# Kernel tuning notes

Hardware: AMD Instinct MI355X
Metric: run time of the kernel (lower is better)

The kernel has to match this reference:

```python
import jax, jax.numpy as jnp
import numpy as np

EMBED = 1024
D_FF = 4 * EMBED
N_EXPERTS = 8
TOP_K = 2
B, S = 2, 1024


def setup_inputs() -> dict:
    key = jax.random.key(0)
    ks = jax.random.split(key, 10)
    sc_d = 1.0 / np.sqrt(EMBED)
    sc_h = 1.0 / np.sqrt(D_FF)
    return {
        "inputs": jax.random.normal(ks[0], (B, S, EMBED), jnp.float32),
        # router MLP: Linear(D,4D) -> ReLU -> Linear(4D,E)
        "rw1": jax.random.normal(ks[1], (EMBED, D_FF), jnp.float32) * sc_d,
        "rb1": jnp.zeros((D_FF,), jnp.float32),
        "rw2": jax.random.normal(ks[2], (D_FF, N_EXPERTS), jnp.float32) * sc_h,
        "rb2": jnp.zeros((N_EXPERTS,), jnp.float32),
        # stacked expert weights: Linear(D,4D) -> ReLU -> Linear(4D,D)
        "W1": jax.random.normal(ks[3], (N_EXPERTS, EMBED, D_FF), jnp.float32) * sc_d,
        "b1": jnp.zeros((N_EXPERTS, D_FF), jnp.float32),
        "W2": jax.random.normal(ks[4], (N_EXPERTS, D_FF, EMBED), jnp.float32) * sc_h,
        "b2": jnp.zeros((N_EXPERTS, EMBED), jnp.float32),
    }


def reference(inputs, rw1, rb1, rw2, rb2, W1, b1, W2, b2):
    Bb, Ss, D = inputs.shape
    T = Bb * Ss
    xf = inputs.reshape(T, D)  # [T, D]

    # Router: scores over experts, keep top-k, softmax over kept entries only.
    score = jax.nn.relu(xf @ rw1 + rb1) @ rw2 + rb2          # [T, E]
    _, topi = jax.lax.top_k(score, TOP_K)                    # [T, K]
    mask = jnp.zeros(score.shape, bool).at[jnp.arange(T)[:, None], topi].set(True)
    gate = jax.nn.softmax(jnp.where(mask, score, -jnp.inf), axis=-1)  # [T, E]

    # Dense per-expert MLP weighted by gate; gate==0 for non-top-k experts,
    # matching the original masked gather/scatter exactly.
    out = jnp.zeros_like(xf)
    for e in range(N_EXPERTS):
        h = jax.nn.relu(xf @ W1[e] + b1[e])                  # [T, 4D]
        y = h @ W2[e] + b2[e]                                # [T, D]
        out = out + gate[:, e:e + 1] * y
    return out.reshape(Bb, Ss, D)
```

## Files before the change

kernel.cpp:

```cpp
#include <hip/hip_runtime.h>
#include <stdint.h>

typedef unsigned short ushort_t;
typedef __attribute__((ext_vector_type(8))) short short8;
typedef __attribute__((ext_vector_type(4))) float f32x4;

#define EMBED   1024
#define DFF     4096
#define NEXP    8
#define TOKENS  2048
#define SLOTS   4096
#define TMAX    40

__device__ __forceinline__ ushort_t f2bf(float f) {
  unsigned u = __float_as_uint(f);
  u += 0x7FFFu + ((u >> 16) & 1u);
  return (ushort_t)(u >> 16);
}
__device__ __forceinline__ float bf2f(ushort_t b) {
  return __uint_as_float(((unsigned)b) << 16);
}

__device__ __forceinline__ void gl2lds16(const void* g, void* l) {
  typedef const __attribute__((address_space(1))) unsigned char* gp_t;
  typedef __attribute__((address_space(3))) unsigned char* lp_t;
  __builtin_amdgcn_global_load_lds((gp_t)(uintptr_t)g, (lp_t)(uintptr_t)l, 16, 0, 0);
}

__global__ void zero_small(int* counts, int* cursors) {
  int i = threadIdx.x;
  if (i < NEXP) { counts[i] = 0; cursors[i] = 0; }
}

__global__ void split_xhl(const float* __restrict__ x, ushort_t* __restrict__ Xs) {
  int t = blockIdx.x;
  int d = threadIdx.x * 4;
  float4 v = *(const float4*)(x + (size_t)t * EMBED + d);
  ushort4 hi, lo;
  hi.x = f2bf(v.x); lo.x = f2bf(v.x - bf2f(hi.x));
  hi.y = f2bf(v.y); lo.y = f2bf(v.y - bf2f(hi.y));
  hi.z = f2bf(v.z); lo.z = f2bf(v.z - bf2f(hi.z));
  hi.w = f2bf(v.w); lo.w = f2bf(v.w - bf2f(hi.w));
  ushort_t* row = Xs + (size_t)t * 2048;
  *(ushort4*)(row + d)        = hi;
  *(ushort4*)(row + 1024 + d) = lo;
}

__global__ void transp_conv(const float* __restrict__ src, ushort_t* __restrict__ dst,
                            int src_ld, int dst_ld, long src_estride, long dst_estride,
                            int dst_koff, int lo)
{
  __shared__ float t[64][65];
  const float* s = src + (size_t)blockIdx.z * src_estride;
  ushort_t* d = dst + (size_t)blockIdx.z * dst_estride;
  int n0 = blockIdx.x * 64, k0 = blockIdx.y * 64;
  int tid = threadIdx.x;
  int kk = tid >> 4, nn = (tid & 15) * 4;
  #pragma unroll
  for (int it = 0; it < 4; it++) {
    float4 v = *(const float4*)(s + (size_t)(k0 + kk + it * 16) * src_ld + n0 + nn);
    t[kk + it * 16][nn]     = v.x;
    t[kk + it * 16][nn + 1] = v.y;
    t[kk + it * 16][nn + 2] = v.z;
    t[kk + it * 16][nn + 3] = v.w;
  }
  __syncthreads();
  int nn2 = tid >> 3, kk2 = (tid & 7) * 8;
  #pragma unroll
  for (int it = 0; it < 2; it++) {
    int n = nn2 + it * 32;
    union { ushort_t u[8]; uint4 v; } pk;
    #pragma unroll
    for (int j = 0; j < 8; j++) {
      float xv = t[kk2 + j][n];
      ushort_t hv = f2bf(xv);
      pk.u[j] = lo ? f2bf(xv - bf2f(hv)) : hv;
    }
    *(uint4*)(d + (size_t)(n0 + n) * dst_ld + dst_koff + k0 + kk2) = pk.v;
  }
}

template<int APATH, int OUTMODE, bool RELU, bool EXPERT, int SPLITK, int NX>
__global__ __launch_bounds__(256, 3)
void gemm_kernel(const ushort_t* __restrict__ A, const ushort_t* __restrict__ B,
                 const float* __restrict__ bias, void* __restrict__ Cout,
                 const float* __restrict__ slot_gate, const int* __restrict__ slot_token,
                 const int* __restrict__ off, const int* __restrict__ tile_e,
                 const int* __restrict__ tile_y, int e0, int e1,
                 int M, int N, int K)
{
  __shared__ ushort_t As[2][128 * 32];
  __shared__ ushort_t Bs[2][128 * 32];

  int e = 0, kc = 0, row0, col0, m_base, m_cnt;
  if (EXPERT) {
    int bid  = blockIdx.x;
    int xi   = bid % NX;
    int rest = bid / NX;
    kc       = rest % SPLITK;
    int t    = rest / SPLITK;
    e = tile_e[t];
    if (e < e0 || e >= e1) return;
    row0   = tile_y[t] * 128;
    col0   = xi * 128;
    m_base = off[e];
    m_cnt  = off[e + 1] - m_base;
  } else {
    row0 = blockIdx.y * 128;
    col0 = blockIdx.x * 128;
    m_base = 0; m_cnt = M;
    if (row0 >= m_cnt) return;
  }
  const int Kc   = K / SPLITK;
  const int kbeg = kc * Kc;

  const int tid  = threadIdx.x;
  const int lane = tid & 63;
  const int wid  = tid >> 6;
  const int wm = wid & 1, wn = wid >> 1;

  const int srow  = lane >> 2;
  const int schk8 = ((lane & 3) ^ ((lane >> 3) & 3)) * 8;

  const ushort_t* gA[2];
  const ushort_t* gB[2];
  int aoff[2];
  const ushort_t* Bt = B + (EXPERT ? (size_t)(e - e0) * (size_t)N * K : 0);
  #pragma unroll
  for (int h = 0; h < 2; h++) {
    int r  = row0 + h * 64 + wid * 16 + srow;
    int rl = min(r, m_cnt - 1);
    size_t rowb;
    if (APATH == 2)      rowb = (size_t)slot_token[m_base + rl] * 2048;
    else if (APATH == 1) rowb = (size_t)rl * 2048;
    else                 rowb = (size_t)(m_base + rl) * (size_t)K;
    gA[h]   = A + rowb + (APATH == 0 ? kbeg : 0) + schk8;
    aoff[h] = (h * 64 + wid * 16) * 32;

    int n = col0 + h * 64 + wid * 16 + srow;
    gB[h] = Bt + (size_t)n * K + kbeg + schk8;
  }

  auto stage = [&](int pb, int k0) {
    const int k0a = (APATH == 1 && k0 >= 2048) ? k0 - 2048 : k0;
    #pragma unroll
    for (int h = 0; h < 2; h++) {
      gl2lds16(gA[h] + k0a, &As[pb][aoff[h]]);
      gl2lds16(gB[h] + k0,  &Bs[pb][aoff[h]]);
    }
  };

  f32x4 acc[4][4];
  #pragma unroll
  for (int i = 0; i < 4; i++)
    #pragma unroll
    for (int j = 0; j < 4; j++)
      acc[i][j] = (f32x4){0.f, 0.f, 0.f, 0.f};

  const int q  = lane >> 4;
  const int rr = lane & 15;
  const int sw8 = (q ^ ((rr >> 1) & 3)) * 8;
  const int abase = (wm * 64 + rr) * 32 + sw8;
  const int bbase = (wn * 64 + rr) * 32 + sw8;

  const int nkt = Kc >> 5;

  stage(0, 0);
  __syncthreads();

  for (int kt = 0; kt < nkt; kt++) {
    const int cur = kt & 1, nxt = cur ^ 1;
    if (kt + 1 < nkt) stage(nxt, (kt + 1) << 5);

    short8 af[4], bfr[4];
    #pragma unroll
    for (int i = 0; i < 4; i++) {
      af[i]  = *(const short8*)(&As[cur][abase + i * 512]);
      bfr[i] = *(const short8*)(&Bs[cur][bbase + i * 512]);
    }
    #pragma unroll
    for (int mt = 0; mt < 4; mt++)
      #pragma unroll
      for (int nt = 0; nt < 4; nt++)
        acc[mt][nt] = __builtin_amdgcn_mfma_f32_16x16x32_bf16(af[mt], bfr[nt], acc[mt][nt], 0, 0, 0);

    __syncthreads();
  }

  const float* biasp = bias + (EXPERT ? (size_t)e * N : 0);
  float bv[4];
  #pragma unroll
  for (int nt = 0; nt < 4; nt++)
    bv[nt] = biasp[col0 + wn * 64 + nt * 16 + rr];
  const float bscale = (SPLITK == 1 || kc == 0) ? 1.f : 0.f;

  if constexpr (OUTMODE == 4) {
    const float* rw2p = slot_gate;
    float4 wa[4], wb[4];
    #pragma unroll
    for (int nt = 0; nt < 4; nt++) {
      int c = col0 + wn * 64 + nt * 16 + rr;
      wa[nt] = *(const float4*)(rw2p + (size_t)c * 8);
      wb[nt] = *(const float4*)(rw2p + (size_t)c * 8 + 4);
    }
    float* Ps = (float*)Cout;
    const int xi2 = (col0 >> 6) + wn;
    #pragma unroll
    for (int mt = 0; mt < 4; mt++) {
      #pragma unroll
      for (int i = 0; i < 4; i++) {
        float4 sA = {0.f, 0.f, 0.f, 0.f}, sB = {0.f, 0.f, 0.f, 0.f};
        #pragma unroll
        for (int nt = 0; nt < 4; nt++) {
          float v = acc[mt][nt][i] + bv[nt];
          if (RELU) v = fmaxf(v, 0.f);
          sA.x += v * wa[nt].x; sA.y += v * wa[nt].y;
          sA.z += v * wa[nt].z; sA.w += v * wa[nt].w;
          sB.x += v * wb[nt].x; sB.y += v * wb[nt].y;
          sB.z += v * wb[nt].z; sB.w += v * wb[nt].w;
        }
        #pragma unroll
        for (int o = 1; o <= 8; o <<= 1) {
          sA.x += __shfl_xor(sA.x, o); sA.y += __shfl_xor(sA.y, o);
          sA.z += __shfl_xor(sA.z, o); sA.w += __shfl_xor(sA.w, o);
          sB.x += __shfl_xor(sB.x, o); sB.y += __shfl_xor(sB.y, o);
          sB.z += __shfl_xor(sB.z, o); sB.w += __shfl_xor(sB.w, o);
        }
        if (rr == 0) {
          int row = row0 + wm * 64 + mt * 16 + q * 4 + i;
          float* p = Ps + ((size_t)row * 64 + xi2) * 8;
          *(float4*)p       = sA;
          *(float4*)(p + 4) = sB;
        }
      }
    }
  } else {
    #pragma unroll
    for (int mt = 0; mt < 4; mt++) {
      #pragma unroll
      for (int i = 0; i < 4; i++) {
        int r_loc = row0 + wm * 64 + mt * 16 + q * 4 + i;
        if (r_loc < m_cnt) {
          int slot = m_base + r_loc;
          float g = 1.f;
          if (OUTMODE == 3) g = slot_gate[slot];
          #pragma unroll
          for (int nt = 0; nt < 4; nt++) {
            float v = acc[mt][nt][i] + bscale * bv[nt];
            if (RELU) v = fmaxf(v, 0.f);
            int c = col0 + wn * 64 + nt * 16 + rr;
            if (OUTMODE == 0)      ((float*)Cout)[(size_t)slot * N + c]    = v;
            else if (OUTMODE == 1) ((ushort_t*)Cout)[(size_t)slot * N + c] = f2bf(v);
            else ((float*)Cout)[((size_t)kc * SLOTS + slot) * N + c] = g * v;
          }
        }
      }
    }
  }
}

__global__ void router_reduce(const float* __restrict__ Ps, const float* __restrict__ rb2,
                              int* __restrict__ topi, float* __restrict__ gates,
                              int* __restrict__ counts)
{
  int t = blockIdx.x * 4 + (threadIdx.x >> 6);
  if (t >= TOKENS) return;
  int lane = threadIdx.x & 63;
  const float* pt = Ps + (size_t)t * 512;
  float4 v0 = *(const float4*)(pt + lane * 8);
  float4 v1 = *(const float4*)(pt + lane * 8 + 4);
  #pragma unroll
  for (int o = 1; o <= 32; o <<= 1) {
    v0.x += __shfl_xor(v0.x, o); v0.y += __shfl_xor(v0.y, o);
    v0.z += __shfl_xor(v0.z, o); v0.w += __shfl_xor(v0.w, o);
    v1.x += __shfl_xor(v1.x, o); v1.y += __shfl_xor(v1.y, o);
    v1.z += __shfl_xor(v1.z, o); v1.w += __shfl_xor(v1.w, o);
  }
  if (lane == 0) {
    float s[8] = {v0.x + rb2[0], v0.y + rb2[1], v0.z + rb2[2], v0.w + rb2[3],
                  v1.x + rb2[4], v1.y + rb2[5], v1.z + rb2[6], v1.w + rb2[7]};
    int i0 = 0;
    #pragma unroll
    for (int e = 1; e < 8; e++) if (s[e] > s[i0]) i0 = e;
    int i1 = (i0 == 0) ? 1 : 0;
    #pragma unroll
    for (int e = 0; e < 8; e++) if (e != i0 && s[e] > s[i1]) i1 = e;
    float ex = __expf(s[i1] - s[i0]);
    float g0 = 1.f / (1.f + ex);
    float g1 = ex / (1.f + ex);
    topi[t * 2] = i0; topi[t * 2 + 1] = i1;
    gates[t * 2] = g0; gates[t * 2 + 1] = g1;
    atomicAdd(&counts[i0], 1);
    atomicAdd(&counts[i1], 1);
  }
}

__global__ void prefix_off(const int* __restrict__ counts, int* __restrict__ off,
                           int* __restrict__ tile_e, int* __restrict__ tile_y)
{
  if (threadIdx.x == 0) {
    int a = 0, t = 0;
    for (int e = 0; e < NEXP; e++) {
      off[e] = a;
      int c = counts[e]; a += c;
      int ty = (c + 127) >> 7;
      for (int y = 0; y < ty; y++) { tile_e[t] = e; tile_y[t] = y; t++; }
    }
    off[NEXP] = a;
    for (; t < TMAX; t++) { tile_e[t] = -1; tile_y[t] = 0; }
  }
}

__global__ void assign_slots(const int* __restrict__ topi, const float* __restrict__ gates,
                             const int* __restrict__ off, int* __restrict__ cursors,
                             int* __restrict__ slot_token, float* __restrict__ slot_gate,
                             int* __restrict__ tok_slot)
{
  int t = blockIdx.x * blockDim.x + threadIdx.x;
  if (t >= TOKENS) return;
  #pragma unroll
  for (int k = 0; k < 2; k++) {
    int e = topi[t * 2 + k];
    int p = atomicAdd(&cursors[e], 1);
    int s = off[e] + p;
    slot_token[s] = t;
    slot_gate[s]  = gates[t * 2 + k];
    tok_slot[t * 2 + k] = s;
  }
}

__global__ void combine_out(const float* __restrict__ Ys, const int* __restrict__ tok_slot,
                            float* __restrict__ out)
{
  int t = blockIdx.x;
  int d = threadIdx.x * 4;
  int s0 = tok_slot[t * 2], s1 = tok_slot[t * 2 + 1];
  float4 a = *(const float4*)(Ys + (size_t)s0 * EMBED + d);
  float4 b = *(const float4*)(Ys + ((size_t)SLOTS + s0) * EMBED + d);
  float4 c = *(const float4*)(Ys + (size_t)s1 * EMBED + d);
  float4 e = *(const float4*)(Ys + ((size_t)SLOTS + s1) * EMBED + d);
  float4 o;
  o.x = (a.x + b.x) + (c.x + e.x);
  o.y = (a.y + b.y) + (c.y + e.y);
  o.z = (a.z + b.z) + (c.z + e.z);
  o.w = (a.w + b.w) + (c.w + e.w);
  *(float4*)(out + (size_t)t * EMBED + d) = o;
}

extern "C" void kernel_launch(void* const* d_in, const int* in_sizes, int n_in,
                              void* d_out, int out_size, void* d_ws, size_t ws_size,
                              hipStream_t stream)
{
  const float* x   = (const float*)d_in[0];
  const float* rw1 = (const float*)d_in[1];
  const float* rb1 = (const float*)d_in[2];
  const float* rw2 = (const float*)d_in[3];
  const float* rb2 = (const float*)d_in[4];
  const float* W1  = (const float*)d_in[5];
  const float* b1  = (const float*)d_in[6];
  const float* W2  = (const float*)d_in[7];
  const float* b2  = (const float*)d_in[8];
  float* out = (float*)d_out;
  char* ws = (char*)d_ws;

  const size_t SZ_R = (size_t)4096 * 4096 * 2;

  ushort_t* RW1t = (ushort_t*)ws;
  ushort_t* WT   = (ushort_t*)ws;
  ushort_t* Hs   = (ushort_t*)(ws + SZ_R);
  ushort_t* Xhl  = (ushort_t*)(ws + 2 * SZ_R);
  float*    Ys   = (float*)(ws + 2 * SZ_R);
  char* ps = ws + 3 * SZ_R;
  float* Ps         = (float*)ps;  ps += (size_t)TOKENS * 512 * 4;
  int*   topi       = (int*)ps;    ps += TOKENS * 2 * 4;
  float* gates      = (float*)ps;  ps += TOKENS * 2 * 4;
  int*   tok_slot   = (int*)ps;    ps += TOKENS * 2 * 4;
  int*   slot_token = (int*)ps;    ps += SLOTS * 4;
  float* slot_gate  = (float*)ps;  ps += SLOTS * 4;
  int*   counts     = (int*)ps;    ps += 256;
  int*   cursors    = (int*)ps;    ps += 256;
  int*   off        = (int*)ps;    ps += 256;
  int*   tile_e     = (int*)ps;    ps += 256;
  int*   tile_y     = (int*)ps;    ps += 256;

  zero_small<<<1, 64, 0, stream>>>(counts, cursors);
  split_xhl<<<TOKENS, 256, 0, stream>>>(x, Xhl);

  transp_conv<<<dim3(64, 16, 1), 256, 0, stream>>>(rw1, RW1t, DFF, 3072, 0, 0, 0,    0);
  transp_conv<<<dim3(64, 16, 1), 256, 0, stream>>>(rw1, RW1t, DFF, 3072, 0, 0, 1024, 0);
  transp_conv<<<dim3(64, 16, 1), 256, 0, stream>>>(rw1, RW1t, DFF, 3072, 0, 0, 2048, 1);

  gemm_kernel<1, 4, true, false, 1, 32>
      <<<dim3(32, 16, 1), 256, 0, stream>>>(Xhl, RW1t, rb1, Ps, rw2, nullptr,
                                            nullptr, nullptr, nullptr, 0, NEXP,
                                            TOKENS, DFF, 3072);
  router_reduce<<<512, 256, 0, stream>>>(Ps, rb2, topi, gates, counts);
  prefix_off  <<<1, 64, 0, stream>>>(counts, off, tile_e, tile_y);
  assign_slots<<<8, 256, 0, stream>>>(topi, gates, off, cursors, slot_token, slot_gate, tok_slot);

  const long W1ES = (long)EMBED * DFF;
  const long W2ES = (long)DFF * EMBED;

  for (int half = 0; half < 2; half++) {
    int e0 = half * 4;
    transp_conv<<<dim3(64, 16, 4), 256, 0, stream>>>(W1 + (size_t)e0 * W1ES, WT,
        DFF, EMBED, W1ES, W1ES, 0, 0);
    gemm_kernel<2, 1, true, true, 1, 32>
        <<<dim3(32 * TMAX, 1, 1), 256, 0, stream>>>(Xhl, WT, b1, Hs,
            nullptr, slot_token, off, tile_e, tile_y, e0, e0 + 4, 0, DFF, EMBED);
  }
  for (int half = 0; half < 2; half++) {
    int e0 = half * 4;
    transp_conv<<<dim3(16, 64, 4), 256, 0, stream>>>(W2 + (size_t)e0 * W2ES, WT,
        EMBED, DFF, W2ES, W2ES, 0, 0);
    gemm_kernel<0, 3, false, true, 2, 8>
        <<<dim3(8 * 2 * TMAX, 1, 1), 256, 0, stream>>>(Hs, WT, b2, Ys,
            slot_gate, nullptr, off, tile_e, tile_y, e0, e0 + 4, 0, EMBED, DFF);
  }

  combine_out<<<TOKENS, 256, 0, stream>>>(Ys, tok_slot, out);
}
```

Measured before the change: 619.7 us.

## Process all experts in single launches when workspace allows, split-K 4 for W2

When the workspace is large enough, all eight experts' weights are transposed and converted at once into dedicated buffers. Each expert GEMM then runs as one launch over all experts instead of two halves. The second GEMM moves to split-K of 4 with a four-way combine, and occupancy hints rise to 4 blocks per CU for the non-router GEMMs. This removes launch serialization and the under-filled half-expert grids, at the cost of more workspace, more split-K partial traffic, and register pressure from the higher occupancy bound.

```diff
diff --git a/kernel.cpp b/kernel.cpp
--- a/kernel.cpp
+++ b/kernel.cpp
@@ -81,7 +81,7 @@
 }
 
 template<int APATH, int OUTMODE, bool RELU, bool EXPERT, int SPLITK, int NX>
-__global__ __launch_bounds__(256, 3)
+__global__ __launch_bounds__(256, (OUTMODE == 4 ? 3 : 4))
 void gemm_kernel(const ushort_t* __restrict__ A, const ushort_t* __restrict__ B,
                  const float* __restrict__ bias, void* __restrict__ Cout,
                  const float* __restrict__ slot_gate, const int* __restrict__ slot_token,
@@ -329,21 +329,23 @@
   }
 }
 
+template<int NC>
 __global__ void combine_out(const float* __restrict__ Ys, const int* __restrict__ tok_slot,
                             float* __restrict__ out)
 {
   int t = blockIdx.x;
   int d = threadIdx.x * 4;
   int s0 = tok_slot[t * 2], s1 = tok_slot[t * 2 + 1];
-  float4 a = *(const float4*)(Ys + (size_t)s0 * EMBED + d);
-  float4 b = *(const float4*)(Ys + ((size_t)SLOTS + s0) * EMBED + d);
-  float4 c = *(const float4*)(Ys + (size_t)s1 * EMBED + d);
-  float4 e = *(const float4*)(Ys + ((size_t)SLOTS + s1) * EMBED + d);
-  float4 o;
-  o.x = (a.x + b.x) + (c.x + e.x);
-  o.y = (a.y + b.y) + (c.y + e.y);
-  o.z = (a.z + b.z) + (c.z + e.z);
-  o.w = (a.w + b.w) + (c.w + e.w);
+  float4 o = {0.f, 0.f, 0.f, 0.f};
+  #pragma unroll
+  for (int k = 0; k < NC; k++) {
+    float4 a = *(const float4*)(Ys + ((size_t)k * SLOTS + s0) * EMBED + d);
+    float4 b = *(const float4*)(Ys + ((size_t)k * SLOTS + s1) * EMBED + d);
+    o.x += a.x + b.x;
+    o.y += a.y + b.y;
+    o.z += a.z + b.z;
+    o.w += a.w + b.w;
+  }
   *(float4*)(out + (size_t)t * EMBED + d) = o;
 }
 
@@ -363,60 +365,109 @@
   float* out = (float*)d_out;
   char* ws = (char*)d_ws;
 
-  const size_t SZ_R = (size_t)4096 * 4096 * 2;
-
-  ushort_t* RW1t = (ushort_t*)ws;
-  ushort_t* WT   = (ushort_t*)ws;
-  ushort_t* Hs   = (ushort_t*)(ws + SZ_R);
-  ushort_t* Xhl  = (ushort_t*)(ws + 2 * SZ_R);
-  float*    Ys   = (float*)(ws + 2 * SZ_R);
-  char* ps = ws + 3 * SZ_R;
-  float* Ps         = (float*)ps;  ps += (size_t)TOKENS * 512 * 4;
-  int*   topi       = (int*)ps;    ps += TOKENS * 2 * 4;
-  float* gates      = (float*)ps;  ps += TOKENS * 2 * 4;
-  int*   tok_slot   = (int*)ps;    ps += TOKENS * 2 * 4;
-  int*   slot_token = (int*)ps;    ps += SLOTS * 4;
-  float* slot_gate  = (float*)ps;  ps += SLOTS * 4;
-  int*   counts     = (int*)ps;    ps += 256;
-  int*   cursors    = (int*)ps;    ps += 256;
-  int*   off        = (int*)ps;    ps += 256;
-  int*   tile_e     = (int*)ps;    ps += 256;
-  int*   tile_y     = (int*)ps;    ps += 256;
-
-  zero_small<<<1, 64, 0, stream>>>(counts, cursors);
-  split_xhl<<<TOKENS, 256, 0, stream>>>(x, Xhl);
-
-  transp_conv<<<dim3(64, 16, 1), 256, 0, stream>>>(rw1, RW1t, DFF, 3072, 0, 0, 0,    0);
-  transp_conv<<<dim3(64, 16, 1), 256, 0, stream>>>(rw1, RW1t, DFF, 3072, 0, 0, 1024, 0);
-  transp_conv<<<dim3(64, 16, 1), 256, 0, stream>>>(rw1, RW1t, DFF, 3072, 0, 0, 2048, 1);
-
-  gemm_kernel<1, 4, true, false, 1, 32>
-      <<<dim3(32, 16, 1), 256, 0, stream>>>(Xhl, RW1t, rb1, Ps, rw2, nullptr,
-                                            nullptr, nullptr, nullptr, 0, NEXP,
-                                            TOKENS, DFF, 3072);
-  router_reduce<<<512, 256, 0, stream>>>(Ps, rb2, topi, gates, counts);
-  prefix_off  <<<1, 64, 0, stream>>>(counts, off, tile_e, tile_y);
-  assign_slots<<<8, 256, 0, stream>>>(topi, gates, off, cursors, slot_token, slot_gate, tok_slot);
-
   const long W1ES = (long)EMBED * DFF;
   const long W2ES = (long)DFF * EMBED;
-
-  for (int half = 0; half < 2; half++) {
-    int e0 = half * 4;
-    transp_conv<<<dim3(64, 16, 4), 256, 0, stream>>>(W1 + (size_t)e0 * W1ES, WT,
-        DFF, EMBED, W1ES, W1ES, 0, 0);
+  const size_t SZ_R = (size_t)4096 * 4096 * 2;
+
+  const bool FULL = ws_size >= ((size_t)300 << 20);
+
+  if (FULL) {
+    char* p = ws;
+    ushort_t* W1T  = (ushort_t*)p;  p += (size_t)NEXP * DFF * EMBED * 2;
+    ushort_t* W2T  = (ushort_t*)p;  p += (size_t)NEXP * EMBED * DFF * 2;
+    ushort_t* RW1t = (ushort_t*)p;  p += (size_t)4096 * 3072 * 2;
+    ushort_t* Hs   = (ushort_t*)p;  p += (size_t)SLOTS * DFF * 2;
+    ushort_t* Xhl  = (ushort_t*)p;  p += (size_t)TOKENS * 2048 * 2;
+    float*    Ys   = (float*)p;     p += (size_t)4 * SLOTS * EMBED * 4;
+    float*    Ps   = (float*)p;     p += (size_t)TOKENS * 512 * 4;
+    int*   topi       = (int*)p;    p += TOKENS * 2 * 4;
+    float* gates      = (float*)p;  p += TOKENS * 2 * 4;
+    int*   tok_slot   = (int*)p;    p += TOKENS * 2 * 4;
+    int*   slot_token = (int*)p;    p += SLOTS * 4;
+    float* slot_gate  = (float*)p;  p += SLOTS * 4;
+    int*   counts     = (int*)p;    p += 256;
+    int*   cursors    = (int*)p;    p += 256;
+    int*   off        = (int*)p;    p += 256;
+    int*   tile_e     = (int*)p;    p += 256;
+    int*   tile_y     = (int*)p;    p += 256;
+
+    zero_small<<<1, 64, 0, stream>>>(counts, cursors);
+    split_xhl<<<TOKENS, 256, 0, stream>>>(x, Xhl);
+
+    transp_conv<<<dim3(64, 16, 1), 256, 0, stream>>>(rw1, RW1t, DFF, 3072, 0, 0, 0,    0);
+    transp_conv<<<dim3(64, 16, 1), 256, 0, stream>>>(rw1, RW1t, DFF, 3072, 0, 0, 1024, 0);
+    transp_conv<<<dim3(64, 16, 1), 256, 0, stream>>>(rw1, RW1t, DFF, 3072, 0, 0, 2048, 1);
+
+    gemm_kernel<1, 4, true, false, 1, 32>
+        <<<dim3(32, 16, 1), 256, 0, stream>>>(Xhl, RW1t, rb1, Ps, rw2, nullptr,
+                                              nullptr, nullptr, nullptr, 0, NEXP,
+                                              TOKENS, DFF, 3072);
+    router_reduce<<<512, 256, 0, stream>>>(Ps, rb2, topi, gates, counts);
+    prefix_off  <<<1, 64, 0, stream>>>(counts, off, tile_e, tile_y);
+    assign_slots<<<8, 256, 0, stream>>>(topi, gates, off, cursors, slot_token, slot_gate, tok_slot);
+
+    transp_conv<<<dim3(64, 16, 8), 256, 0, stream>>>(W1, W1T, DFF, EMBED, W1ES, W1ES, 0, 0);
     gemm_kernel<2, 1, true, true, 1, 32>
-        <<<dim3(32 * TMAX, 1, 1), 256, 0, stream>>>(Xhl, WT, b1, Hs,
-            nullptr, slot_token, off, tile_e, tile_y, e0, e0 + 4, 0, DFF, EMBED);
-  }
-  for (int half = 0; half < 2; half++) {
-    int e0 = half * 4;
-    transp_conv<<<dim3(16, 64, 4), 256, 0, stream>>>(W2 + (size_t)e0 * W2ES, WT,
-        EMBED, DFF, W2ES, W2ES, 0, 0);
-    gemm_kernel<0, 3, false, true, 2, 8>
-        <<<dim3(8 * 2 * TMAX, 1, 1), 256, 0, stream>>>(Hs, WT, b2, Ys,
-            slot_gate, nullptr, off, tile_e, tile_y, e0, e0 + 4, 0, EMBED, DFF);
-  }
-
-  combine_out<<<TOKENS, 256, 0, stream>>>(Ys, tok_slot, out);
-}
+        <<<dim3(32 * TMAX, 1, 1), 256, 0, stream>>>(Xhl, W1T, b1, Hs,
+            nullptr, slot_token, off, tile_e, tile_y, 0, NEXP, 0, DFF, EMBED);
+
+    transp_conv<<<dim3(16, 64, 8), 256, 0, stream>>>(W2, W2T, EMBED, DFF, W2ES, W2ES, 0, 0);
+    gemm_kernel<0, 3, false, true, 4, 8>
+        <<<dim3(8 * 4 * TMAX, 1, 1), 256, 0, stream>>>(Hs, W2T, b2, Ys,
+            slot_gate, nullptr, off, tile_e, tile_y, 0, NEXP, 0, EMBED, DFF);
+
+    combine_out<4><<<TOKENS, 256, 0, stream>>>(Ys, tok_slot, out);
+  } else {
+    ushort_t* RW1t = (ushort_t*)ws;
+    ushort_t* WT   = (ushort_t*)ws;
+    ushort_t* Hs   = (ushort_t*)(ws + SZ_R);
+    ushort_t* Xhl  = (ushort_t*)(ws + 2 * SZ_R);
+    float*    Ys   = (float*)(ws + 2 * SZ_R);
+    char* p = ws + 3 * SZ_R;
+    float* Ps         = (float*)p;  p += (size_t)TOKENS * 512 * 4;
+    int*   topi       = (int*)p;    p += TOKENS * 2 * 4;
+    float* gates      = (float*)p;  p += TOKENS * 2 * 4;
+    int*   tok_slot   = (int*)p;    p += TOKENS * 2 * 4;
+    int*   slot_token = (int*)p;    p += SLOTS * 4;
+    float* slot_gate  = (float*)p;  p += SLOTS * 4;
+    int*   counts     = (int*)p;    p += 256;
+    int*   cursors    = (int*)p;    p += 256;
+    int*   off        = (int*)p;    p += 256;
+    int*   tile_e     = (int*)p;    p += 256;
+    int*   tile_y     = (int*)p;    p += 256;
+
+    zero_small<<<1, 64, 0, stream>>>(counts, cursors);
+    split_xhl<<<TOKENS, 256, 0, stream>>>(x, Xhl);
+
+    transp_conv<<<dim3(64, 16, 1), 256, 0, stream>>>(rw1, RW1t, DFF, 3072, 0, 0, 0,    0);
+    transp_conv<<<dim3(64, 16, 1), 256, 0, stream>>>(rw1, RW1t, DFF, 3072, 0, 0, 1024, 0);
+    transp_conv<<<dim3(64, 16, 1), 256, 0, stream>>>(rw1, RW1t, DFF, 3072, 0, 0, 2048, 1);
+
+    gemm_kernel<1, 4, true, false, 1, 32>
+        <<<dim3(32, 16, 1), 256, 0, stream>>>(Xhl, RW1t, rb1, Ps, rw2, nullptr,
+                                              nullptr, nullptr, nullptr, 0, NEXP,
+                                              TOKENS, DFF, 3072);
+    router_reduce<<<512, 256, 0, stream>>>(Ps, rb2, topi, gates, counts);
+    prefix_off  <<<1, 64, 0, stream>>>(counts, off, tile_e, tile_y);
+    assign_slots<<<8, 256, 0, stream>>>(topi, gates, off, cursors, slot_token, slot_gate, tok_slot);
+
+    for (int half = 0; half < 2; half++) {
+      int e0 = half * 4;
+      transp_conv<<<dim3(64, 16, 4), 256, 0, stream>>>(W1 + (size_t)e0 * W1ES, WT,
+          DFF, EMBED, W1ES, W1ES, 0, 0);
+      gemm_kernel<2, 1, true, true, 1, 32>
+          <<<dim3(32 * TMAX, 1, 1), 256, 0, stream>>>(Xhl, WT, b1, Hs,
+              nullptr, slot_token, off, tile_e, tile_y, e0, e0 + 4, 0, DFF, EMBED);
+    }
+    for (int half = 0; half < 2; half++) {
+      int e0 = half * 4;
+      transp_conv<<<dim3(16, 64, 4), 256, 0, stream>>>(W2 + (size_t)e0 * W2ES, WT,
+          EMBED, DFF, W2ES, W2ES, 0, 0);
+      gemm_kernel<0, 3, false, true, 2, 8>
+          <<<dim3(8 * 2 * TMAX, 1, 1), 256, 0, stream>>>(Hs, WT, b2, Ys,
+              slot_gate, nullptr, off, tile_e, tile_y, e0, e0 + 4, 0, EMBED, DFF);
+    }
+
+    combine_out<2><<<TOKENS, 256, 0, stream>>>(Ys, tok_slot, out);
+  }
+}
```

New measurement: 621.0 us. About the same (+0.2%).
